# Optimization experiments

Measured on AMD Instinct MI355X. Metric: run time of the kernel, lower is better.

## Reference

```python
import jax, jax.numpy as jnp
import numpy as np

N = 512          # max_nodes
H = 256          # hidden_dim
L = 4            # num_layers
T = 100          # num_timesteps
NE = N * (N - 1) // 2  # 130816 upper-triangular edges

# --- cosine noise schedule (computed in float64 numpy, stored as float32) ---
_s = 0.008
_steps = np.arange(T + 1, dtype=np.float64)
_ab = np.cos((_steps / T + _s) / (1 + _s) * np.pi / 2) ** 2
_ab = _ab / _ab[0]
_betas = np.clip(1.0 - _ab[1:] / _ab[:-1], None, 0.999).astype(np.float32)
_alphas = 1.0 - _betas
_alpha_bar = np.cumprod(_alphas).astype(np.float32)
SQRT_AB = jnp.asarray(np.sqrt(_alpha_bar), dtype=jnp.float32)
SQRT_OMAB = jnp.asarray(np.sqrt(1.0 - _alpha_bar), dtype=jnp.float32)
IU, JU = np.triu_indices(N, k=1)  # upper-triangular edge indices


def silu(x):
    return x * jax.nn.sigmoid(x)


def layernorm(x, g, b, eps=1e-5):
    mu = jnp.mean(x, axis=-1, keepdims=True)
    var = jnp.mean(jnp.square(x - mu), axis=-1, keepdims=True)
    return (x - mu) / jnp.sqrt(var + eps) * g + b


def setup_inputs() -> dict:
    key = jax.random.key(0)
    ks = jax.random.split(key, 16)
    B = 32
    p = lambda k, shape: jax.random.normal(k, shape, dtype=jnp.float32) * 0.02
    return {
        "adj_0": jax.random.normal(ks[0], (B, N, N), dtype=jnp.float32),
        "noise": jax.random.normal(ks[1], (B, N, N), dtype=jnp.float32),
        # time embedding MLP: Linear(1,H), SiLU, Linear(H,H)
        "te_W1": p(ks[2], (1, H)), "te_b1": jnp.zeros((H,), jnp.float32),
        "te_W2": p(ks[3], (H, H)), "te_b2": jnp.zeros((H,), jnp.float32),
        # input projection Linear(N, H)
        "ip_W": p(ks[4], (N, H)), "ip_b": jnp.zeros((H,), jnp.float32),
        # per-layer params stacked on leading L axis
        "msg_W": p(ks[5], (L, H, H)), "msg_b": jnp.zeros((L, H), jnp.float32),
        "upd_W": p(ks[6], (L, 2 * H, H)), "upd_b": jnp.zeros((L, H), jnp.float32),
        "ln_g": jnp.ones((L, H), jnp.float32), "ln_b": jnp.zeros((L, H), jnp.float32),
        "tp_W": p(ks[7], (L, H, H)), "tp_b": jnp.zeros((L, H), jnp.float32),
        # output projection: Linear(H,H), SiLU, Linear(H, NE)
        "op_W1": p(ks[8], (H, H)), "op_b1": jnp.zeros((H,), jnp.float32),
        "op_W2": p(ks[9], (H, NE)), "op_b2": jnp.zeros((NE,), jnp.float32),
        "t": jax.random.randint(ks[10], (32,), 0, T),
    }


def reference(adj_0, noise, te_W1, te_b1, te_W2, te_b2, ip_W, ip_b,
              msg_W, msg_b, upd_W, upd_b, ln_g, ln_b, tp_W, tp_b,
              op_W1, op_b1, op_W2, op_b2, t):
    # q_sample: noisy adjacency at timestep t
    adj_t = SQRT_AB[t][:, None, None] * adj_0 + SQRT_OMAB[t][:, None, None] * noise
    # time embedding
    tf = (t.astype(jnp.float32) / T)[:, None]               # [B,1]
    t_emb = silu(tf @ te_W1 + te_b1) @ te_W2 + te_b2        # [B,H]
    # input projection
    h = adj_t @ ip_W + ip_b                                  # [B,N,H]
    # adjacency normalization is identical across layers -> hoist
    adj_norm = adj_t / (jnp.sum(jnp.abs(adj_t), axis=-1, keepdims=True) + 1.0)
    for l in range(L):
        msg = jnp.einsum('bij,bjh->bih', adj_norm, h @ msg_W[l] + msg_b[l])
        t_bias = (t_emb @ tp_W[l] + tp_b[l])[:, None, :]     # [B,1,H]
        h_new = jnp.concatenate([h, msg], axis=-1) @ upd_W[l] + upd_b[l] + t_bias
        h = layernorm(h_new + h, ln_g[l], ln_b[l])
    h_graph = jnp.sum(h, axis=1)                             # [B,H]
    noise_pred = silu(h_graph @ op_W1 + op_b1) @ op_W2 + op_b2  # [B,NE]
    # MSE against the upper-triangular entries of the true noise
    target = noise[:, IU, JU]                                # [B,NE]
    loss = jnp.mean(jnp.square(noise_pred - target))
    return loss
```

## Files before the change

kernel.cpp:

```cpp
#include <hip/hip_runtime.h>
#include <math.h>

#define NN 512
#define HH 256
#define BB 32
#define NE 130816

typedef unsigned short ushort_t;
typedef unsigned int u32;
using short8  = __attribute__((ext_vector_type(8))) short;
using floatx4 = __attribute__((ext_vector_type(4))) float;

typedef __attribute__((address_space(3))) u32* lds_u32p;
typedef const __attribute__((address_space(1))) u32* glb_u32p;

__device__ inline unsigned short f2bf(float f) {
    unsigned int u = __float_as_uint(f);
    unsigned int r = (u + 0x7fffu + ((u >> 16) & 1u)) >> 16;
    return (unsigned short)r;
}
__device__ inline float bf2f(unsigned short x) {
    return __uint_as_float(((unsigned int)x) << 16);
}

__device__ inline float wave_reduce_sum(float v) {
#pragma unroll
    for (int o = 32; o > 0; o >>= 1) v += __shfl_xor(v, o, 64);
    return v;
}
__device__ inline float block_reduce_sum256(float v, float* red) {
    v = wave_reduce_sum(v);
    int w = threadIdx.x >> 6;
    if ((threadIdx.x & 63) == 0) red[w] = v;
    __syncthreads();
    v = red[0] + red[1] + red[2] + red[3];
    __syncthreads();
    return v;
}

__global__ void init_kernel(float* __restrict__ sched, float* __restrict__ out) {
    __shared__ float alpha_s[100];
    int tid = threadIdx.x;
    if (tid < 100) {
        const double PI_H = 3.14159265358979323846 * 0.5;
        double f1 = (((double)tid / 100.0) + 0.008) / 1.008 * PI_H;
        double f2 = (((double)(tid + 1) / 100.0) + 0.008) / 1.008 * PI_H;
        double c1 = cos(f1), c2 = cos(f2);
        double beta = 1.0 - (c2 * c2) / (c1 * c1);
        if (beta > 0.999) beta = 0.999;
        alpha_s[tid] = 1.0f - (float)beta;
    }
    __syncthreads();
    if (tid == 0) {
        out[0] = 0.0f;
        float cum = 1.0f;
        for (int k = 0; k < 100; k++) {
            cum *= alpha_s[k];
            sched[k]       = sqrtf(cum);
            sched[100 + k] = sqrtf(1.0f - cum);
        }
    }
}

__global__ __launch_bounds__(256) void temb1_kernel(
    const float* __restrict__ te_W1, const float* __restrict__ te_b1,
    const float* __restrict__ te_W2, const float* __restrict__ te_b2,
    const int* __restrict__ t, float* __restrict__ emb_out) {
    const int b = blockIdx.x, cb = blockIdx.y * 64, tid = threadIdx.x;
    __shared__ float hid[HH];
    __shared__ float part[4][64];
    float tf = (float)t[b] / 100.0f;
    float z = tf * te_W1[tid] + te_b1[tid];
    hid[tid] = z / (1.0f + expf(-z));
    __syncthreads();
    const int col = tid & 63, kc = tid >> 6;
    float a = 0.0f;
#pragma unroll 8
    for (int k0 = 0; k0 < 64; k0++) {
        int k = kc * 64 + k0;
        a = fmaf(hid[k], te_W2[k * HH + cb + col], a);
    }
    part[kc][col] = a;
    __syncthreads();
    if (kc == 0) {
        float o = part[0][col] + part[1][col] + part[2][col] + part[3][col] + te_b2[cb + col];
        emb_out[b * HH + cb + col] = o;
    }
}

__global__ __launch_bounds__(256) void temb2_kernel(
    const float* __restrict__ emb, const float* __restrict__ tp_W,
    const float* __restrict__ tp_b, float* __restrict__ tbias_out) {
    const int b = blockIdx.x;
    const int l = blockIdx.y >> 2, cb = (blockIdx.y & 3) * 64;
    const int tid = threadIdx.x;
    __shared__ float es[HH];
    __shared__ float part[4][64];
    es[tid] = emb[b * HH + tid];
    __syncthreads();
    const int col = tid & 63, kc = tid >> 6;
    const float* W = tp_W + l * HH * HH;
    float a = 0.0f;
#pragma unroll 8
    for (int k0 = 0; k0 < 64; k0++) {
        int k = kc * 64 + k0;
        a = fmaf(es[k], W[k * HH + cb + col], a);
    }
    part[kc][col] = a;
    __syncthreads();
    if (kc == 0) {
        float o = part[0][col] + part[1][col] + part[2][col] + part[3][col]
                + tp_b[l * HH + cb + col];
        tbias_out[l * (BB * HH) + b * HH + cb + col] = o;
    }
}

__global__ __launch_bounds__(256) void adj_kernel(
    const float* __restrict__ adj0, const float* __restrict__ noise,
    const int* __restrict__ t, const float* __restrict__ sched,
    ushort_t* __restrict__ adjt_bf, float* __restrict__ invrs) {
    __shared__ float red[4];
    const int bid = blockIdx.x;
    const int b = bid >> 9;
    const int ts = t[b];
    const float sab = sched[ts], som = sched[100 + ts];
    const size_t base = (size_t)bid * NN;
    const int tid = threadIdx.x;
    const int j = tid * 2;
    float2 a0 = *(const float2*)&adj0[base + j];
    float2 n0 = *(const float2*)&noise[base + j];
    float x = fmaf(sab, a0.x, som * n0.x);
    float y = fmaf(sab, a0.y, som * n0.y);
    *(u32*)&adjt_bf[base + j] = (u32)f2bf(x) | ((u32)f2bf(y) << 16);
    float s = fabsf(x) + fabsf(y);
    s = block_reduce_sum256(s, red);
    if (tid == 0) invrs[bid] = 1.0f / (s + 1.0f);
}

__global__ __launch_bounds__(256) void wcvt_kernel(
    const float* __restrict__ ip_W, const float* __restrict__ msg_W,
    const float* __restrict__ upd_W,
    ushort_t* __restrict__ ipWT, ushort_t* __restrict__ msgWbf,
    ushort_t* __restrict__ updWT) {
    const int z = blockIdx.z;
    const int r0 = blockIdx.y * 32, c0 = blockIdx.x * 32;
    const int tr = threadIdx.x >> 5, tc = threadIdx.x & 31;
    if (z >= 1 && z <= 4) {
        const float* src = msg_W + (z - 1) * 65536;
        ushort_t* dst = msgWbf + (z - 1) * 65536;
        if (r0 >= 256) return;
#pragma unroll
        for (int s = 0; s < 32; s += 8)
            dst[(size_t)(r0 + tr + s) * 256 + c0 + tc] =
                f2bf(src[(size_t)(r0 + tr + s) * 256 + c0 + tc]);
        return;
    }
    const float* src; ushort_t* dst; int R;
    if (z == 0) { src = ip_W;                     dst = ipWT;                     R = 512; }
    else        { src = upd_W + (z - 5) * 131072; dst = updWT + (z - 5) * 131072; R = 512; }
    __shared__ float T[32][33];
#pragma unroll
    for (int s = 0; s < 32; s += 8)
        T[tr + s][tc] = src[(size_t)(r0 + tr + s) * 256 + c0 + tc];
    __syncthreads();
#pragma unroll
    for (int s = 0; s < 32; s += 8)
        dst[(size_t)(c0 + tr + s) * R + r0 + tc] = f2bf(T[tc][tr + s]);
}

__global__ __launch_bounds__(256) void bfv_kernel(
    const float* __restrict__ msg_b, const float* __restrict__ upd_W,
    float* __restrict__ bfv) {
    const int l = blockIdx.x, n = threadIdx.x;
    float a = 0.0f;
#pragma unroll 8
    for (int j = 0; j < 256; j++)
        a = fmaf(msg_b[l * 256 + j], upd_W[(size_t)l * 131072 + (size_t)(256 + j) * 256 + n], a);
    bfv[l * 256 + n] = a;
}

__global__ __launch_bounds__(256, 2) void gemm_bf16(
    int K, int nsplit,
    const ushort_t* __restrict__ A, int lda, long long aStrideZ,
    const ushort_t* __restrict__ BT, int ldbt,
    const ushort_t* __restrict__ BT2, int ldbt2,
    long long btStrideZ, long long bstride,
    const float* __restrict__ bias, const float* __restrict__ bias2,
    const float* __restrict__ scale,
    const float* __restrict__ tbias, const ushort_t* __restrict__ resid,
    const ushort_t* __restrict__ part1,
    float* __restrict__ Cf, ushort_t* __restrict__ Cb, ushort_t* __restrict__ CbT,
    long long cStrideZ) {
    __shared__ ushort_t As[128 * 32];
    __shared__ ushort_t Bs[64 * 32];
    __shared__ ushort_t Ts[64 * 136];
    const int row0 = blockIdx.x * 128;
    const int n0 = blockIdx.y * 64;
    const int z = blockIdx.z;
    const int tid = threadIdx.x;
    const int lane = tid & 63;
    const int w = tid >> 6;
    const int l15 = lane & 15, quad = lane >> 4;
    const int wm = (w >> 1) * 64, wn = (w & 1) * 32;

    const bool reg2 = (n0 >= nsplit);
    const ushort_t* BTu = reg2 ? BT2 : BT;
    const int ldbtu = reg2 ? ldbt2 : ldbt;
    const int n0u = reg2 ? (n0 - nsplit) : n0;
    const ushort_t* Az = A + (size_t)z * aStrideZ;
    const ushort_t* Bp = BTu + (size_t)z * btStrideZ + (size_t)(row0 >> 9) * (size_t)bstride;

    const int srow = lane >> 2;
    const int gkoff = (((lane & 3) ^ (lane >> 4)) << 3);
    const int swz = ((quad ^ ((l15 >> 2) & 3)) << 3);

    floatx4 acc[4][2];
#pragma unroll
    for (int i = 0; i < 4; i++)
#pragma unroll
        for (int j = 0; j < 2; j++) {
            acc[i][j][0] = 0.0f; acc[i][j][1] = 0.0f;
            acc[i][j][2] = 0.0f; acc[i][j][3] = 0.0f;
        }

    for (int kc = 0; kc < K; kc += 32) {
#pragma unroll
        for (int r = 0; r < 2; r++) {
            const int lbase = (r * 4 + w) * 16;
            const ushort_t* gpA = Az + (size_t)(row0 + lbase + srow) * lda + kc + gkoff;
            __builtin_amdgcn_global_load_lds((glb_u32p)(const void*)gpA,
                                             (lds_u32p)(void*)&As[lbase * 32], 16, 0, 0);
        }
        {
            const int lbase = w * 16;
            const ushort_t* gpB = Bp + (size_t)(n0u + lbase + srow) * ldbtu + kc + gkoff;
            __builtin_amdgcn_global_load_lds((glb_u32p)(const void*)gpB,
                                             (lds_u32p)(void*)&Bs[lbase * 32], 16, 0, 0);
        }
        __syncthreads();

        short8 af[4], bfr[2];
#pragma unroll
        for (int tm = 0; tm < 4; tm++)
            af[tm] = *(const short8*)&As[(wm + tm * 16 + l15) * 32 + swz];
#pragma unroll
        for (int tn = 0; tn < 2; tn++)
            bfr[tn] = *(const short8*)&Bs[(wn + tn * 16 + l15) * 32 + swz];
#pragma unroll
        for (int tm = 0; tm < 4; tm++)
#pragma unroll
            for (int tn = 0; tn < 2; tn++)
                acc[tm][tn] = __builtin_amdgcn_mfma_f32_16x16x32_bf16(
                    af[tm], bfr[tn], acc[tm][tn], 0, 0, 0);
        __syncthreads();
    }

    if (reg2) {
#pragma unroll
        for (int tm = 0; tm < 4; tm++)
#pragma unroll
            for (int tn = 0; tn < 2; tn++)
#pragma unroll
                for (int r = 0; r < 4; r++) {
                    const int ml = wm + tm * 16 + quad * 4 + r;
                    const int cl = wn + tn * 16 + l15;
                    float v = acc[tm][tn][r];
                    if (bias2) v += bias2[n0u + cl];
                    Ts[cl * 136 + ml] = f2bf(v);
                }
        __syncthreads();
        const int cl = tid >> 2, ch = (tid & 3) * 32;
        const int b = row0 >> 9;
        ushort_t* dst = CbT + (size_t)b * NN * HH + (size_t)(n0u + cl) * NN + (row0 & 511) + ch;
        uint4 u0 = *(const uint4*)&Ts[cl * 136 + ch];
        uint4 u1 = *(const uint4*)&Ts[cl * 136 + ch + 8];
        uint4 u2 = *(const uint4*)&Ts[cl * 136 + ch + 16];
        uint4 u3 = *(const uint4*)&Ts[cl * 136 + ch + 24];
        *(uint4*)(dst)      = u0;
        *(uint4*)(dst + 8)  = u1;
        *(uint4*)(dst + 16) = u2;
        *(uint4*)(dst + 24) = u3;
        return;
    }

#pragma unroll
    for (int tm = 0; tm < 4; tm++)
#pragma unroll
        for (int tn = 0; tn < 2; tn++) {
#pragma unroll
            for (int r = 0; r < 4; r++) {
                const int row = row0 + wm + tm * 16 + quad * 4 + r;
                const int col = n0 + wn + tn * 16 + l15;
                float v = acc[tm][tn][r];
                if (scale) v *= scale[row];
                if (bias) v += bias[col];
                if (part1) v += bf2f(part1[(size_t)row * HH + col]);
                if (tbias) v += tbias[((row >> 9) << 8) + col] + bf2f(resid[(size_t)row * HH + col]);
                if (Cf) Cf[(size_t)row * HH + col] = v;
                if (Cb) Cb[(size_t)z * cStrideZ + (size_t)row * HH + col] = f2bf(v);
            }
        }
}

__global__ __launch_bounds__(256) void ln_kernel(
    const float* __restrict__ pre, const float* __restrict__ g,
    const float* __restrict__ b, ushort_t* __restrict__ h_bf) {
    __shared__ float red[4];
    const size_t base = (size_t)blockIdx.x * HH;
    const int tid = threadIdx.x;
    float x = pre[base + tid];
    float mu = block_reduce_sum256(x, red) * (1.0f / HH);
    float d = x - mu;
    float var = block_reduce_sum256(d * d, red) * (1.0f / HH);
    h_bf[base + tid] = f2bf(d * rsqrtf(var + 1e-5f) * g[tid] + b[tid]);
}

__global__ __launch_bounds__(256) void psum_kernel(
    const ushort_t* __restrict__ h_bf, float* __restrict__ partial) {
    const int b = blockIdx.x, ch = blockIdx.y, tid = threadIdx.x;
    const ushort_t* hp = h_bf + ((size_t)b * NN + ch * 32) * HH;
    float s = 0.0f;
#pragma unroll
    for (int i = 0; i < 32; i++) s += bf2f(hp[i * HH + tid]);
    partial[(((size_t)b * 16 + ch) << 8) + tid] = s;
}

__global__ __launch_bounds__(256) void final_kernel(
    const float* __restrict__ partial, const float* __restrict__ op_W1,
    const float* __restrict__ op_b1, float* __restrict__ sT) {
    int b = blockIdx.x, tid = threadIdx.x;
    __shared__ float hg[HH];
    float acc = 0.0f;
#pragma unroll
    for (int c = 0; c < 16; c++) acc += partial[(((size_t)b * 16 + c) << 8) + tid];
    hg[tid] = acc;
    __syncthreads();
    float o = op_b1[tid];
#pragma unroll 8
    for (int k = 0; k < HH; k++) o = fmaf(hg[k], op_W1[k * HH + tid], o);
    sT[tid * BB + b] = o / (1.0f + expf(-o));
}

__global__ __launch_bounds__(256) void loss_kernel(
    const float* __restrict__ sT, const float* __restrict__ op_W2,
    const float* __restrict__ op_b2, const float* __restrict__ noise,
    float* __restrict__ out) {
    __shared__ float red[4];
    const int tid = threadIdx.x;
    const int e = blockIdx.x * 256 + tid;
    float lsum = 0.0f;
    float acc[32];
#pragma unroll
    for (int b = 0; b < 32; b++) acc[b] = 0.0f;
    const float* w2 = op_W2 + e;
#pragma unroll 8
    for (int h = 0; h < 256; h++) {
        float wv = w2[(size_t)h * NE];
        const float* sr = sT + h * BB;
#pragma unroll
        for (int b = 0; b < 32; b++) acc[b] = fmaf(sr[b], wv, acc[b]);
    }
    int i = (int)((1023.0 - sqrt(1046529.0 - 8.0 * (double)e)) * 0.5);
    if (i < 0) i = 0;
    if (i > 510) i = 510;
    while (i > 0 && (i * (1023 - i)) / 2 > e) --i;
    while (((i + 1) * (1022 - i)) / 2 <= e) ++i;
    int j = i + 1 + (e - (i * (1023 - i)) / 2);
    const float pb = op_b2[e];
    const float* np = noise + (size_t)i * NN + j;
#pragma unroll
    for (int b = 0; b < 32; b++) {
        float d = acc[b] + pb - np[(size_t)b * NN * NN];
        lsum += d * d;
    }
    lsum *= (1.0f / (32.0f * (float)NE));
    lsum = block_reduce_sum256(lsum, red);
    if (tid == 0) atomicAdd(out, lsum);
}

extern "C" void kernel_launch(void* const* d_in, const int* in_sizes, int n_in,
                              void* d_out, int out_size, void* d_ws, size_t ws_size,
                              hipStream_t stream) {
    const float* adj0  = (const float*)d_in[0];
    const float* noise = (const float*)d_in[1];
    const float* te_W1 = (const float*)d_in[2];
    const float* te_b1 = (const float*)d_in[3];
    const float* te_W2 = (const float*)d_in[4];
    const float* te_b2 = (const float*)d_in[5];
    const float* ip_W  = (const float*)d_in[6];
    const float* ip_b  = (const float*)d_in[7];
    const float* msg_W = (const float*)d_in[8];
    const float* msg_b = (const float*)d_in[9];
    const float* upd_W = (const float*)d_in[10];
    const float* upd_b = (const float*)d_in[11];
    const float* ln_g  = (const float*)d_in[12];
    const float* ln_b  = (const float*)d_in[13];
    const float* tp_W  = (const float*)d_in[14];
    const float* tp_b  = (const float*)d_in[15];
    const float* op_W1 = (const float*)d_in[16];
    const float* op_b1 = (const float*)d_in[17];
    const float* op_W2 = (const float*)d_in[18];
    const float* op_b2 = (const float*)d_in[19];
    const int*   t     = (const int*)d_in[20];
    float* out = (float*)d_out;

    float* ws = (float*)d_ws;
    float* sched   = ws;
    float* tbias   = ws + 256;
    float* invrs   = ws + 33024;
    float* sbuf    = ws + 49408;
    float* embb    = ws + 57600;
    float* bfv     = ws + 65792;
    float* partial = ws + 66816;
    float* pre     = ws + 197888;
    ushort_t* bfb  = (ushort_t*)(ws + 4392192);
    ushort_t* adjt_bf = bfb;
    ushort_t* h_bf    = bfb + 8388608;
    ushort_t* part1   = bfb + 12582912;
    ushort_t* hm2T    = bfb + 16777216;
    ushort_t* ipWT    = bfb + 20971520;
    ushort_t* msgWbf  = bfb + 21102592;
    ushort_t* updWT   = bfb + 21364736;
    ushort_t* WfT     = bfb + 21889024;

    const int NS_OFF = 1 << 30;

    init_kernel<<<1, 128, 0, stream>>>(sched, out);
    wcvt_kernel<<<dim3(8, 16, 9), 256, 0, stream>>>(ip_W, msg_W, upd_W, ipWT, msgWbf, updWT);
    bfv_kernel<<<4, 256, 0, stream>>>(msg_b, upd_W, bfv);
    temb1_kernel<<<dim3(32, 4), 256, 0, stream>>>(te_W1, te_b1, te_W2, te_b2, t, embb);
    temb2_kernel<<<dim3(32, 16), 256, 0, stream>>>(embb, tp_W, tp_b, tbias);
    adj_kernel<<<BB * NN, 256, 0, stream>>>(adj0, noise, t, sched, adjt_bf, invrs);

    gemm_bf16<<<dim3(2, 4, 4), 256, 0, stream>>>(
        256, NS_OFF,
        updWT + 256, 512, 131072,
        msgWbf, 256, nullptr, 0, 65536, 0,
        nullptr, nullptr, nullptr, nullptr, nullptr, nullptr,
        nullptr, WfT, nullptr, 65536);

    gemm_bf16<<<dim3(128, 4), 256, 0, stream>>>(
        512, NS_OFF,
        adjt_bf, 512, 0,
        ipWT, 512, nullptr, 0, 0, 0,
        ip_b, nullptr, nullptr, nullptr, nullptr, nullptr,
        nullptr, h_bf, nullptr, 0);

    for (int l = 0; l < 4; l++) {
        gemm_bf16<<<dim3(128, 8), 256, 0, stream>>>(
            256, 256,
            h_bf, 256, 0,
            updWT + l * 131072, 512,
            WfT + l * 65536, 256, 0, 0,
            nullptr, bfv + l * 256, nullptr, nullptr, nullptr, nullptr,
            nullptr, part1, hm2T, 0);
        gemm_bf16<<<dim3(128, 4), 256, 0, stream>>>(
            512, NS_OFF,
            adjt_bf, 512, 0,
            hm2T, 512, nullptr, 0, 0, (long long)(HH * NN),
            upd_b + l * HH, nullptr, invrs,
            tbias + l * BB * HH, h_bf, part1,
            pre, nullptr, nullptr, 0);
        ln_kernel<<<BB * NN, 256, 0, stream>>>(pre, ln_g + l * HH, ln_b + l * HH, h_bf);
    }
    psum_kernel<<<dim3(32, 16), 256, 0, stream>>>(h_bf, partial);
    final_kernel<<<32, 256, 0, stream>>>(partial, op_W1, op_b1, sbuf);
    loss_kernel<<<511, 256, 0, stream>>>(sbuf, op_W2, op_b2, noise, out);
}
```

Measured before the change: 636.3 us.

## Load GEMM fragments directly from global, use per-wave rows in adj and layernorm

The bf16 GEMM drops LDS staging and barriers. Each wave now loads its MFMA A/B fragments straight from global memory, with K as a template parameter so the loop fully unrolls. The adj and layernorm kernels now give one row to each wave, using wide vector loads and shuffle-only reductions, and layernorm uses a single pass with E[x^2]-mu^2. The loss kernel's unroll is raised. In exchange, operand tiles shared between waves in a block are no longer reused through LDS and are fetched redundantly via cache. The single-pass variance is also slightly less numerically robust.

```diff
diff --git a/kernel.cpp b/kernel.cpp
--- a/kernel.cpp
+++ b/kernel.cpp
@@ -10,9 +10,6 @@
 typedef unsigned int u32;
 using short8  = __attribute__((ext_vector_type(8))) short;
 using floatx4 = __attribute__((ext_vector_type(4))) float;
-
-typedef __attribute__((address_space(3))) u32* lds_u32p;
-typedef const __attribute__((address_space(1))) u32* glb_u32p;
 
 __device__ inline unsigned short f2bf(float f) {
     unsigned int u = __float_as_uint(f);
@@ -119,22 +116,30 @@
     const float* __restrict__ adj0, const float* __restrict__ noise,
     const int* __restrict__ t, const float* __restrict__ sched,
     ushort_t* __restrict__ adjt_bf, float* __restrict__ invrs) {
-    __shared__ float red[4];
-    const int bid = blockIdx.x;
-    const int b = bid >> 9;
+    const int row = blockIdx.x * 4 + (threadIdx.x >> 6);
+    const int lane = threadIdx.x & 63;
+    const int b = row >> 9;
     const int ts = t[b];
     const float sab = sched[ts], som = sched[100 + ts];
-    const size_t base = (size_t)bid * NN;
-    const int tid = threadIdx.x;
-    const int j = tid * 2;
-    float2 a0 = *(const float2*)&adj0[base + j];
-    float2 n0 = *(const float2*)&noise[base + j];
-    float x = fmaf(sab, a0.x, som * n0.x);
-    float y = fmaf(sab, a0.y, som * n0.y);
-    *(u32*)&adjt_bf[base + j] = (u32)f2bf(x) | ((u32)f2bf(y) << 16);
-    float s = fabsf(x) + fabsf(y);
-    s = block_reduce_sum256(s, red);
-    if (tid == 0) invrs[bid] = 1.0f / (s + 1.0f);
+    const size_t base = (size_t)row * NN + lane * 8;
+    float4 a0 = *(const float4*)(adj0 + base);
+    float4 a1 = *(const float4*)(adj0 + base + 4);
+    float4 q0 = *(const float4*)(noise + base);
+    float4 q1 = *(const float4*)(noise + base + 4);
+    float v0 = fmaf(sab, a0.x, som * q0.x), v1 = fmaf(sab, a0.y, som * q0.y);
+    float v2 = fmaf(sab, a0.z, som * q0.z), v3 = fmaf(sab, a0.w, som * q0.w);
+    float v4 = fmaf(sab, a1.x, som * q1.x), v5 = fmaf(sab, a1.y, som * q1.y);
+    float v6 = fmaf(sab, a1.z, som * q1.z), v7 = fmaf(sab, a1.w, som * q1.w);
+    uint4 pk;
+    pk.x = (u32)f2bf(v0) | ((u32)f2bf(v1) << 16);
+    pk.y = (u32)f2bf(v2) | ((u32)f2bf(v3) << 16);
+    pk.z = (u32)f2bf(v4) | ((u32)f2bf(v5) << 16);
+    pk.w = (u32)f2bf(v6) | ((u32)f2bf(v7) << 16);
+    *(uint4*)(adjt_bf + base) = pk;
+    float s = fabsf(v0) + fabsf(v1) + fabsf(v2) + fabsf(v3)
+            + fabsf(v4) + fabsf(v5) + fabsf(v6) + fabsf(v7);
+    s = wave_reduce_sum(s);
+    if (lane == 0) invrs[row] = 1.0f / (s + 1.0f);
 }
 
 __global__ __launch_bounds__(256) void wcvt_kernel(
@@ -179,8 +184,9 @@
     bfv[l * 256 + n] = a;
 }
 
-__global__ __launch_bounds__(256, 2) void gemm_bf16(
-    int K, int nsplit,
+template<int K>
+__global__ __launch_bounds__(256) void gemm_nolds(
+    int nsplit,
     const ushort_t* __restrict__ A, int lda, long long aStrideZ,
     const ushort_t* __restrict__ BT, int ldbt,
     const ushort_t* __restrict__ BT2, int ldbt2,
@@ -191,8 +197,6 @@
     const ushort_t* __restrict__ part1,
     float* __restrict__ Cf, ushort_t* __restrict__ Cb, ushort_t* __restrict__ CbT,
     long long cStrideZ) {
-    __shared__ ushort_t As[128 * 32];
-    __shared__ ushort_t Bs[64 * 32];
     __shared__ ushort_t Ts[64 * 136];
     const int row0 = blockIdx.x * 128;
     const int n0 = blockIdx.y * 64;
@@ -207,12 +211,18 @@
     const ushort_t* BTu = reg2 ? BT2 : BT;
     const int ldbtu = reg2 ? ldbt2 : ldbt;
     const int n0u = reg2 ? (n0 - nsplit) : n0;
-    const ushort_t* Az = A + (size_t)z * aStrideZ;
-    const ushort_t* Bp = BTu + (size_t)z * btStrideZ + (size_t)(row0 >> 9) * (size_t)bstride;
-
-    const int srow = lane >> 2;
-    const int gkoff = (((lane & 3) ^ (lane >> 4)) << 3);
-    const int swz = ((quad ^ ((l15 >> 2) & 3)) << 3);
+
+    const ushort_t* Abase = A + (size_t)z * aStrideZ
+                            + (size_t)(row0 + wm + l15) * lda + quad * 8;
+    const ushort_t* Bbase = BTu + (size_t)z * btStrideZ
+                            + (size_t)(row0 >> 9) * (size_t)bstride
+                            + (size_t)(n0u + wn + l15) * ldbtu + quad * 8;
+    const ushort_t* aP0 = Abase;
+    const ushort_t* aP1 = Abase + (size_t)16 * lda;
+    const ushort_t* aP2 = Abase + (size_t)32 * lda;
+    const ushort_t* aP3 = Abase + (size_t)48 * lda;
+    const ushort_t* bP0 = Bbase;
+    const ushort_t* bP1 = Bbase + (size_t)16 * ldbtu;
 
     floatx4 acc[4][2];
 #pragma unroll
@@ -223,36 +233,22 @@
             acc[i][j][2] = 0.0f; acc[i][j][3] = 0.0f;
         }
 
+#pragma unroll
     for (int kc = 0; kc < K; kc += 32) {
-#pragma unroll
-        for (int r = 0; r < 2; r++) {
-            const int lbase = (r * 4 + w) * 16;
-            const ushort_t* gpA = Az + (size_t)(row0 + lbase + srow) * lda + kc + gkoff;
-            __builtin_amdgcn_global_load_lds((glb_u32p)(const void*)gpA,
-                                             (lds_u32p)(void*)&As[lbase * 32], 16, 0, 0);
-        }
-        {
-            const int lbase = w * 16;
-            const ushort_t* gpB = Bp + (size_t)(n0u + lbase + srow) * ldbtu + kc + gkoff;
-            __builtin_amdgcn_global_load_lds((glb_u32p)(const void*)gpB,
-                                             (lds_u32p)(void*)&Bs[lbase * 32], 16, 0, 0);
-        }
-        __syncthreads();
-
-        short8 af[4], bfr[2];
-#pragma unroll
-        for (int tm = 0; tm < 4; tm++)
-            af[tm] = *(const short8*)&As[(wm + tm * 16 + l15) * 32 + swz];
-#pragma unroll
-        for (int tn = 0; tn < 2; tn++)
-            bfr[tn] = *(const short8*)&Bs[(wn + tn * 16 + l15) * 32 + swz];
-#pragma unroll
-        for (int tm = 0; tm < 4; tm++)
-#pragma unroll
-            for (int tn = 0; tn < 2; tn++)
-                acc[tm][tn] = __builtin_amdgcn_mfma_f32_16x16x32_bf16(
-                    af[tm], bfr[tn], acc[tm][tn], 0, 0, 0);
-        __syncthreads();
+        short8 af0 = *(const short8*)(aP0 + kc);
+        short8 af1 = *(const short8*)(aP1 + kc);
+        short8 af2 = *(const short8*)(aP2 + kc);
+        short8 af3 = *(const short8*)(aP3 + kc);
+        short8 bf0 = *(const short8*)(bP0 + kc);
+        short8 bf1 = *(const short8*)(bP1 + kc);
+        acc[0][0] = __builtin_amdgcn_mfma_f32_16x16x32_bf16(af0, bf0, acc[0][0], 0, 0, 0);
+        acc[0][1] = __builtin_amdgcn_mfma_f32_16x16x32_bf16(af0, bf1, acc[0][1], 0, 0, 0);
+        acc[1][0] = __builtin_amdgcn_mfma_f32_16x16x32_bf16(af1, bf0, acc[1][0], 0, 0, 0);
+        acc[1][1] = __builtin_amdgcn_mfma_f32_16x16x32_bf16(af1, bf1, acc[1][1], 0, 0, 0);
+        acc[2][0] = __builtin_amdgcn_mfma_f32_16x16x32_bf16(af2, bf0, acc[2][0], 0, 0, 0);
+        acc[2][1] = __builtin_amdgcn_mfma_f32_16x16x32_bf16(af2, bf1, acc[2][1], 0, 0, 0);
+        acc[3][0] = __builtin_amdgcn_mfma_f32_16x16x32_bf16(af3, bf0, acc[3][0], 0, 0, 0);
+        acc[3][1] = __builtin_amdgcn_mfma_f32_16x16x32_bf16(af3, bf1, acc[3][1], 0, 0, 0);
     }
 
     if (reg2) {
@@ -305,14 +301,28 @@
 __global__ __launch_bounds__(256) void ln_kernel(
     const float* __restrict__ pre, const float* __restrict__ g,
     const float* __restrict__ b, ushort_t* __restrict__ h_bf) {
-    __shared__ float red[4];
-    const size_t base = (size_t)blockIdx.x * HH;
-    const int tid = threadIdx.x;
-    float x = pre[base + tid];
-    float mu = block_reduce_sum256(x, red) * (1.0f / HH);
-    float d = x - mu;
-    float var = block_reduce_sum256(d * d, red) * (1.0f / HH);
-    h_bf[base + tid] = f2bf(d * rsqrtf(var + 1e-5f) * g[tid] + b[tid]);
+    const int row = blockIdx.x * 4 + (threadIdx.x >> 6);
+    const int lane = threadIdx.x & 63;
+    const float* pr = pre + (size_t)row * HH;
+    float4 x = ((const float4*)pr)[lane];
+    float s = x.x + x.y + x.z + x.w;
+    float q = x.x * x.x + x.y * x.y + x.z * x.z + x.w * x.w;
+#pragma unroll
+    for (int o = 32; o > 0; o >>= 1) {
+        s += __shfl_xor(s, o, 64);
+        q += __shfl_xor(q, o, 64);
+    }
+    float mu = s * (1.0f / HH);
+    float var = q * (1.0f / HH) - mu * mu;
+    float rs = rsqrtf(var + 1e-5f);
+    float4 gv = ((const float4*)g)[lane];
+    float4 bv = ((const float4*)b)[lane];
+    uint2 pk;
+    pk.x = (u32)f2bf((x.x - mu) * rs * gv.x + bv.x)
+         | ((u32)f2bf((x.y - mu) * rs * gv.y + bv.y) << 16);
+    pk.y = (u32)f2bf((x.z - mu) * rs * gv.z + bv.z)
+         | ((u32)f2bf((x.w - mu) * rs * gv.w + bv.w) << 16);
+    *(uint2*)(h_bf + (size_t)row * HH + lane * 4) = pk;
 }
 
 __global__ __launch_bounds__(256) void psum_kernel(
@@ -353,7 +363,7 @@
 #pragma unroll
     for (int b = 0; b < 32; b++) acc[b] = 0.0f;
     const float* w2 = op_W2 + e;
-#pragma unroll 8
+#pragma unroll 16
     for (int h = 0; h < 256; h++) {
         float wv = w2[(size_t)h * NE];
         const float* sr = sT + h * BB;
@@ -430,38 +440,38 @@
     bfv_kernel<<<4, 256, 0, stream>>>(msg_b, upd_W, bfv);
     temb1_kernel<<<dim3(32, 4), 256, 0, stream>>>(te_W1, te_b1, te_W2, te_b2, t, embb);
     temb2_kernel<<<dim3(32, 16), 256, 0, stream>>>(embb, tp_W, tp_b, tbias);
-    adj_kernel<<<BB * NN, 256, 0, stream>>>(adj0, noise, t, sched, adjt_bf, invrs);
-
-    gemm_bf16<<<dim3(2, 4, 4), 256, 0, stream>>>(
-        256, NS_OFF,
+    adj_kernel<<<4096, 256, 0, stream>>>(adj0, noise, t, sched, adjt_bf, invrs);
+
+    gemm_nolds<256><<<dim3(2, 4, 4), 256, 0, stream>>>(
+        NS_OFF,
         updWT + 256, 512, 131072,
         msgWbf, 256, nullptr, 0, 65536, 0,
         nullptr, nullptr, nullptr, nullptr, nullptr, nullptr,
         nullptr, WfT, nullptr, 65536);
 
-    gemm_bf16<<<dim3(128, 4), 256, 0, stream>>>(
-        512, NS_OFF,
+    gemm_nolds<512><<<dim3(128, 4), 256, 0, stream>>>(
+        NS_OFF,
         adjt_bf, 512, 0,
         ipWT, 512, nullptr, 0, 0, 0,
         ip_b, nullptr, nullptr, nullptr, nullptr, nullptr,
         nullptr, h_bf, nullptr, 0);
 
     for (int l = 0; l < 4; l++) {
-        gemm_bf16<<<dim3(128, 8), 256, 0, stream>>>(
-            256, 256,
+        gemm_nolds<256><<<dim3(128, 8), 256, 0, stream>>>(
+            256,
             h_bf, 256, 0,
             updWT + l * 131072, 512,
             WfT + l * 65536, 256, 0, 0,
             nullptr, bfv + l * 256, nullptr, nullptr, nullptr, nullptr,
             nullptr, part1, hm2T, 0);
-        gemm_bf16<<<dim3(128, 4), 256, 0, stream>>>(
-            512, NS_OFF,
+        gemm_nolds<512><<<dim3(128, 4), 256, 0, stream>>>(
+            NS_OFF,
             adjt_bf, 512, 0,
             hm2T, 512, nullptr, 0, 0, (long long)(HH * NN),
             upd_b + l * HH, nullptr, invrs,
             tbias + l * BB * HH, h_bf, part1,
             pre, nullptr, nullptr, 0);
-        ln_kernel<<<BB * NN, 256, 0, stream>>>(pre, ln_g + l * HH, ln_b + l * HH, h_bf);
+        ln_kernel<<<4096, 256, 0, stream>>>(pre, ln_g + l * HH, ln_b + l * HH, h_bf);
     }
     psum_kernel<<<dim3(32, 16), 256, 0, stream>>>(h_bf, partial);
     final_kernel<<<32, 256, 0, stream>>>(partial, op_W1, op_b1, sbuf);
```

After: 747.9 us. 17.5% more time.
